# Performance work log

Hardware: AMD Instinct MI355X
Metric: run time of the kernel (lower is better)

Reference implementation:

```python
import jax, jax.numpy as jnp
import numpy as np

LN_EPS = 1e-5


def setup_inputs() -> dict:
    key = jax.random.key(0)
    ks = jax.random.split(key, 8)
    N, E, DIN, DOUT = 50000, 800000, 128, 128
    s = 1.0 / np.sqrt(DIN)
    return {
        "vertex_features": jax.random.normal(ks[0], (N, DIN), jnp.float32),
        "edge_index": jax.random.randint(ks[1], (2, E), 0, N, jnp.int32),
        "W_edge": jax.random.normal(ks[2], (DIN, DOUT), jnp.float32) * s,
        "b_edge": jnp.zeros((DOUT,), jnp.float32),
        "W1": jax.random.normal(ks[3], (DIN + DOUT, DOUT), jnp.float32) * (1.0 / np.sqrt(DIN + DOUT)),
        "b1": jnp.zeros((DOUT,), jnp.float32),
        "ln_gamma": jnp.ones((DOUT,), jnp.float32),
        "ln_beta": jnp.zeros((DOUT,), jnp.float32),
        "W2": jax.random.normal(ks[4], (DOUT, DOUT), jnp.float32) * (1.0 / np.sqrt(DOUT)),
        "b2": jnp.zeros((DOUT,), jnp.float32),
    }


def layer_norm(x, gamma, beta):
    mu = jnp.mean(x, axis=-1, keepdims=True)
    var = jnp.mean(jnp.square(x - mu), axis=-1, keepdims=True)
    return (x - mu) * jax.lax.rsqrt(var + LN_EPS) * gamma + beta


def reference(vertex_features, edge_index, W_edge, b_edge, W1, b1, ln_gamma, ln_beta, W2, b2):
    N = vertex_features.shape[0]
    src, dst = edge_index[0], edge_index[1]
    # gather-subtract: [E, DIN]
    edge_feats = vertex_features[src] - vertex_features[dst]
    # edge linear: [E, DOUT]
    edge_feats = edge_feats @ W_edge + b_edge
    # scatter_max by dst -> [N, DOUT]; empty segments get -inf -> replace with 0
    agg = jax.ops.segment_max(edge_feats, dst, num_segments=N)
    agg = jnp.where(jnp.isfinite(agg), agg, 0.0)
    combined = jnp.concatenate([vertex_features, agg], axis=-1)  # [N, DIN+DOUT]
    h = combined @ W1 + b1
    h = jax.nn.relu(layer_norm(h, ln_gamma, ln_beta))
    return h @ W2 + b2
```

## Files before the change

### kernel.cpp

```cpp
#include <hip/hip_runtime.h>
#include <stdint.h>

#define DIN 128
#define DOUT 128
#define LN_EPS 1e-5f
#define CAP 64

typedef __attribute__((ext_vector_type(8))) short bf16x8;
typedef __attribute__((ext_vector_type(4))) float f32x4;

__device__ __forceinline__ unsigned short f2bf(float f) {
  uint32_t u = __float_as_uint(f);
  uint32_t r = (u + 0x7fffu + ((u >> 16) & 1u)) >> 16;
  return (unsigned short)r;
}
__device__ __forceinline__ float bf2f(uint32_t lo16) {
  return __uint_as_float(lo16 << 16);
}
__device__ __forceinline__ uint32_t pack2(unsigned short a, unsigned short b) {
  return (uint32_t)a | ((uint32_t)b << 16);
}
__device__ __forceinline__ uint32_t cvtpk_bf16(float lo, float hi) {
  uint32_t r;
  asm volatile("v_cvt_pk_bf16_f32 %0, %1, %2" : "=v"(r) : "v"(lo), "v"(hi));
  return r;
}

__global__ __launch_bounds__(256) void k_prep(
    const float* __restrict__ We, const float* __restrict__ W1,
    const float* __restrict__ W2, char* __restrict__ img,
    int4* __restrict__ degv4, int nv4, int wblk) {
  if (blockIdx.x >= wblk) {
    int i = (blockIdx.x - wblk) * 256 + threadIdx.x;
    if (i < nv4) degv4[i] = make_int4(0, 0, 0, 0);
    return;
  }
  int tid = blockIdx.x * 256 + threadIdx.x;
  const int total = 128 * 128 + 256 * 128 + 128 * 128;
  for (int i = tid; i < total; i += wblk * 256) {
    int off;
    float v;
    if (i < 16384) {
      int k = i >> 7, c = i & 127;
      v = We[k * 128 + c];
      off = c * 256 + ((k * 2) ^ ((c & 7) << 4));
    } else if (i < 49152) {
      int j = i - 16384;
      int k = j >> 7, c = j & 127;
      v = W1[k * 128 + c];
      off = 32768 + c * 512 + ((k * 2) ^ ((c & 7) << 4));
    } else {
      int j = i - 49152;
      int k = j >> 7, c = j & 127;
      v = W2[k * 128 + c];
      off = 98304 + c * 256 + ((k * 2) ^ ((c & 7) << 4));
    }
    *(unsigned short*)(img + off) = f2bf(v);
  }
}

__global__ __launch_bounds__(256, 1) void k_gemm_histplace(
    const float* __restrict__ vf, const char* __restrict__ wimg,
    short* __restrict__ P16, short* __restrict__ vf16, int N,
    const int* __restrict__ ei, int* __restrict__ deg,
    unsigned short* __restrict__ ssrc, int E, int nblk) {
  __shared__ char Wet[32768];
  if (blockIdx.x >= nblk) {
    int e = (blockIdx.x - nblk) * 256 + threadIdx.x;
    if (e < E) {
      int s = ei[e];
      int d = ei[E + e];
      int r = atomicAdd(&deg[d], 1);
      if (r < CAP) ssrc[(size_t)d * CAP + r] = (unsigned short)s;
    }
    return;
  }
  {
    const uint4* src = (const uint4*)wimg;
    for (int i = threadIdx.x; i < 2048; i += 256) *(uint4*)(Wet + i * 16) = src[i];
  }
  int wave = threadIdx.x >> 6, lane = threadIdx.x & 63;
  int l15 = lane & 15, lq = lane >> 4;
  int row0 = blockIdx.x * 256 + wave * 64;
  int rs[4];
#pragma unroll
  for (int m = 0; m < 4; ++m) rs[m] = min(row0 + m * 16 + l15, N - 1);

  f32x4 acc[4][8];
#pragma unroll
  for (int m = 0; m < 4; ++m)
#pragma unroll
    for (int n = 0; n < 8; ++n) acc[m][n] = (f32x4)0.f;

  float4 pf0[4], pf1[4];
#pragma unroll
  for (int m = 0; m < 4; ++m) {
    const float* p = vf + (size_t)rs[m] * DIN + lq * 8;
    pf0[m] = *(const float4*)p;
    pf1[m] = *(const float4*)(p + 4);
  }
  __syncthreads();

#pragma unroll
  for (int ks = 0; ks < 4; ++ks) {
    bf16x8 afr[4];
#pragma unroll
    for (int m = 0; m < 4; ++m) {
      uint4 st;
      st.x = cvtpk_bf16(pf0[m].x, pf0[m].y);
      st.y = cvtpk_bf16(pf0[m].z, pf0[m].w);
      st.z = cvtpk_bf16(pf1[m].x, pf1[m].y);
      st.w = cvtpk_bf16(pf1[m].z, pf1[m].w);
      afr[m] = *(bf16x8*)&st;
      int row = row0 + m * 16 + l15;
      if (row < N)
        *(uint4*)(vf16 + (size_t)row * DIN + ks * 32 + lq * 8) = st;
    }
    if (ks < 3) {
#pragma unroll
      for (int m = 0; m < 4; ++m) {
        const float* p = vf + (size_t)rs[m] * DIN + (ks + 1) * 32 + lq * 8;
        pf0[m] = *(const float4*)p;
        pf1[m] = *(const float4*)(p + 4);
      }
    }
    int kb = ks * 64 + lq * 16;
#pragma unroll
    for (int n = 0; n < 8; ++n) {
      int c = n * 16 + l15;
      bf16x8 b = *(const bf16x8*)(Wet + c * 256 + (kb ^ ((c & 7) << 4)));
#pragma unroll
      for (int m = 0; m < 4; ++m)
        acc[m][n] = __builtin_amdgcn_mfma_f32_16x16x32_bf16(afr[m], b, acc[m][n], 0, 0, 0);
    }
  }
#pragma unroll
  for (int m = 0; m < 4; ++m) {
    int rbase = row0 + m * 16 + lq * 4;
#pragma unroll
    for (int n = 0; n < 8; ++n) {
      int col = n * 16 + l15;
#pragma unroll
      for (int reg = 0; reg < 4; ++reg) {
        int row = rbase + reg;
        if (row < N) P16[(size_t)row * DOUT + col] = (short)f2bf(acc[m][n][reg]);
      }
    }
  }
}

__global__ __launch_bounds__(256) void k_segmax(const short* __restrict__ P16,
                                                const int* __restrict__ degA,
                                                const unsigned short* __restrict__ ssrc,
                                                const float* __restrict__ b_edge,
                                                short* __restrict__ A16, int N) {
  int lane = threadIdx.x & 63;
  int l16 = lane & 15;
  int v = blockIdx.x * 16 + (threadIdx.x >> 4);
  if (v >= N) return;
  int deg = min(degA[v], CAP);
  size_t beg = (size_t)v * CAP;
  float m[8];
#pragma unroll
  for (int j = 0; j < 8; ++j) m[j] = -__builtin_inff();
  for (int r = 0; r < deg; r += 16) {
    int cnt = min(16, deg - r);
    int sv = (l16 < cnt) ? (int)ssrc[beg + r + l16] : 0;
#pragma unroll 2
    for (int i = 0; i < cnt; ++i) {
      int s = __shfl(sv, (lane & 48) + i, 64);
      uint4 p = *(const uint4*)(P16 + (size_t)s * DOUT + l16 * 8);
      m[0] = fmaxf(m[0], bf2f(p.x & 0xffffu));
      m[1] = fmaxf(m[1], bf2f(p.x >> 16));
      m[2] = fmaxf(m[2], bf2f(p.y & 0xffffu));
      m[3] = fmaxf(m[3], bf2f(p.y >> 16));
      m[4] = fmaxf(m[4], bf2f(p.z & 0xffffu));
      m[5] = fmaxf(m[5], bf2f(p.z >> 16));
      m[6] = fmaxf(m[6], bf2f(p.w & 0xffffu));
      m[7] = fmaxf(m[7], bf2f(p.w >> 16));
    }
  }
  uint4 pv = *(const uint4*)(P16 + (size_t)v * DOUT + l16 * 8);
  float4 be0 = *(const float4*)(b_edge + l16 * 8);
  float4 be1 = *(const float4*)(b_edge + l16 * 8 + 4);
  float pvf[8] = {bf2f(pv.x & 0xffffu), bf2f(pv.x >> 16), bf2f(pv.y & 0xffffu),
                  bf2f(pv.y >> 16),     bf2f(pv.z & 0xffffu), bf2f(pv.z >> 16),
                  bf2f(pv.w & 0xffffu), bf2f(pv.w >> 16)};
  float bev[8] = {be0.x, be0.y, be0.z, be0.w, be1.x, be1.y, be1.z, be1.w};
  uint32_t o[4];
#pragma unroll
  for (int j = 0; j < 4; ++j) {
    float a0 = (deg > 0) ? (m[2 * j] - pvf[2 * j] + bev[2 * j]) : 0.f;
    float a1 = (deg > 0) ? (m[2 * j + 1] - pvf[2 * j + 1] + bev[2 * j + 1]) : 0.f;
    o[j] = pack2(f2bf(a0), f2bf(a1));
  }
  *(uint4*)(A16 + (size_t)v * DOUT + l16 * 8) = *(uint4*)o;
}

__global__ __launch_bounds__(256, 2) void k_mlp12(
    const short* __restrict__ vf16, const short* __restrict__ A16,
    const char* __restrict__ wimg, const float* __restrict__ b1,
    const float* __restrict__ gamma, const float* __restrict__ beta,
    const float* __restrict__ b2, float* __restrict__ out, int N) {
  __shared__ char lds[65536];
  char* W1h = lds;
  char* W2t = lds + 32768;
  {
    const uint4* wsrc = (const uint4*)wimg;
    for (int i = threadIdx.x; i < 2048; i += 256) {
      int c = i >> 4, x = i & 15;
      ((uint4*)W1h)[i] = wsrc[2048 + c * 32 + x];
      ((uint4*)W2t)[i] = wsrc[6144 + i];
    }
  }
  int wave = threadIdx.x >> 6, lane = threadIdx.x & 63;
  int l15 = lane & 15, lq = lane >> 4;
  int row0 = blockIdx.x * 128 + wave * 32;
  int rs[2];
#pragma unroll
  for (int m = 0; m < 2; ++m) rs[m] = min(row0 + m * 16 + l15, N - 1);
  float b1v[8], gv[8], bev[8], b2v[8];
#pragma unroll
  for (int n = 0; n < 8; ++n) {
    int c = n * 16 + l15;
    b1v[n] = b1[c];
    gv[n] = gamma[c];
    bev[n] = beta[c];
    b2v[n] = b2[c];
  }
  f32x4 acc[2][8];
#pragma unroll
  for (int m = 0; m < 2; ++m)
#pragma unroll
    for (int n = 0; n < 8; ++n) acc[m][n] = (f32x4)0.f;

  uint4 pa[2];
#pragma unroll
  for (int m = 0; m < 2; ++m)
    pa[m] = *(const uint4*)(vf16 + (size_t)rs[m] * DIN + lq * 8);
  __syncthreads();

#pragma unroll
  for (int ks = 0; ks < 8; ++ks) {
    if (ks == 4) {
      __syncthreads();
      const uint4* wsrc = (const uint4*)wimg;
      for (int i = threadIdx.x; i < 2048; i += 256) {
        int c = i >> 4, x = i & 15;
        ((uint4*)W1h)[i] = wsrc[2048 + c * 32 + 16 + x];
      }
      __syncthreads();
    }
    bf16x8 afr[2];
#pragma unroll
    for (int m = 0; m < 2; ++m) afr[m] = *(bf16x8*)&pa[m];
    if (ks < 7) {
      int ks1 = ks + 1;
      const short* srcb = (ks1 < 4) ? vf16 : A16;
      int chunk = (ks1 < 4) ? ks1 : ks1 - 4;
#pragma unroll
      for (int m = 0; m < 2; ++m)
        pa[m] = *(const uint4*)(srcb + (size_t)rs[m] * DIN + chunk * 32 + lq * 8);
    }
    int kb = (ks & 3) * 64 + lq * 16;
#pragma unroll
    for (int n = 0; n < 8; ++n) {
      int c = n * 16 + l15;
      bf16x8 b = *(const bf16x8*)(W1h + c * 256 + (kb ^ ((c & 7) << 4)));
#pragma unroll
      for (int m = 0; m < 2; ++m)
        acc[m][n] = __builtin_amdgcn_mfma_f32_16x16x32_bf16(afr[m], b, acc[m][n], 0, 0, 0);
    }
  }
  __syncthreads();

#pragma unroll
  for (int m = 0; m < 2; ++m) {
#pragma unroll
    for (int n = 0; n < 8; ++n)
#pragma unroll
      for (int reg = 0; reg < 4; ++reg) acc[m][n][reg] += b1v[n];
    float s[4], sq[4];
#pragma unroll
    for (int reg = 0; reg < 4; ++reg) {
      s[reg] = 0.f;
      sq[reg] = 0.f;
#pragma unroll
      for (int n = 0; n < 8; ++n) {
        float h = acc[m][n][reg];
        s[reg] += h;
        sq[reg] += h * h;
      }
    }
#pragma unroll
    for (int mm = 1; mm < 16; mm <<= 1) {
#pragma unroll
      for (int reg = 0; reg < 4; ++reg) {
        s[reg] += __shfl_xor(s[reg], mm, 64);
        sq[reg] += __shfl_xor(sq[reg], mm, 64);
      }
    }
#pragma unroll
    for (int reg = 0; reg < 4; ++reg) {
      float mu = s[reg] * (1.f / 128.f);
      float var = sq[reg] * (1.f / 128.f) - mu * mu;
      float rsn = rsqrtf(var + LN_EPS);
      int rr = wave * 32 + m * 16 + lq * 4 + reg;
#pragma unroll
      for (int n = 0; n < 8; ++n) {
        float o = fmaxf(fmaf((acc[m][n][reg] - mu) * rsn, gv[n], bev[n]), 0.f);
        int c = n * 16 + l15;
        *(unsigned short*)(W1h + rr * 256 + ((c * 2) ^ ((rr & 7) << 4))) = f2bf(o);
      }
    }
  }
  __syncthreads();

  f32x4 acc2[2][8];
#pragma unroll
  for (int m = 0; m < 2; ++m)
#pragma unroll
    for (int n = 0; n < 8; ++n) acc2[m][n] = (f32x4)0.f;
#pragma unroll
  for (int ks = 0; ks < 4; ++ks) {
    int kb = ks * 64 + lq * 16;
    bf16x8 a2[2];
#pragma unroll
    for (int m = 0; m < 2; ++m) {
      int rr = wave * 32 + m * 16 + l15;
      a2[m] = *(const bf16x8*)(W1h + rr * 256 + (kb ^ ((rr & 7) << 4)));
    }
#pragma unroll
    for (int n = 0; n < 8; ++n) {
      int c = n * 16 + l15;
      bf16x8 b = *(const bf16x8*)(W2t + c * 256 + (kb ^ ((c & 7) << 4)));
#pragma unroll
      for (int m = 0; m < 2; ++m)
        acc2[m][n] = __builtin_amdgcn_mfma_f32_16x16x32_bf16(a2[m], b, acc2[m][n], 0, 0, 0);
    }
  }
#pragma unroll
  for (int m = 0; m < 2; ++m) {
    int rbase = row0 + m * 16 + lq * 4;
#pragma unroll
    for (int n = 0; n < 8; ++n) {
      int col = n * 16 + l15;
#pragma unroll
      for (int reg = 0; reg < 4; ++reg) {
        int row = rbase + reg;
        if (row < N) out[(size_t)row * DOUT + col] = acc2[m][n][reg] + b2v[n];
      }
    }
  }
}

extern "C" void kernel_launch(void* const* d_in, const int* in_sizes, int n_in,
                              void* d_out, int out_size, void* d_ws, size_t ws_size,
                              hipStream_t stream) {
  const float* vf     = (const float*)d_in[0];
  const int*   ei     = (const int*)d_in[1];
  const float* W_edge = (const float*)d_in[2];
  const float* b_edge = (const float*)d_in[3];
  const float* W1     = (const float*)d_in[4];
  const float* b1     = (const float*)d_in[5];
  const float* gamma  = (const float*)d_in[6];
  const float* beta   = (const float*)d_in[7];
  const float* W2     = (const float*)d_in[8];
  const float* b2     = (const float*)d_in[9];
  float* out = (float*)d_out;

  int N = in_sizes[0] / DIN;
  int E = in_sizes[1] / 2;
  int nblk = (N + 255) / 256;
  int eblk = (E + 255) / 256;
  int mblk = (N + 127) / 128;

  char* ws = (char*)d_ws;
  size_t seg16 = (size_t)N * DOUT * sizeof(short);
  short* P16  = (short*)ws;
  short* vf16 = (short*)(ws + seg16);
  short* A16  = (short*)(ws + 2 * seg16);
  char*  wimg = ws + 3 * seg16;
  int*   deg  = (int*)(ws + 3 * seg16 + 131072);
  unsigned short* ssrc = (unsigned short*)(deg + ((N + 3) & ~3));

  int nv4 = (N + 3) / 4;
  int zblk = (nv4 + 255) / 256;
  k_prep<<<64 + zblk, 256, 0, stream>>>(W_edge, W1, W2, wimg, (int4*)deg, nv4, 64);
  k_gemm_histplace<<<nblk + eblk, 256, 0, stream>>>(vf, wimg, P16, vf16, N, ei,
                                                    deg, ssrc, E, nblk);
  k_segmax<<<(N + 15) / 16, 256, 0, stream>>>(P16, deg, ssrc, b_edge, A16, N);
  k_mlp12<<<mblk, 256, 0, stream>>>(vf16, A16, wimg, b1, gamma, beta, b2, out, N);
}
```

Measured before the change: 109.3 us.

## Fuse segment-max aggregation into the MLP kernel via shared-memory tile

```diff
diff --git a/kernel.cpp b/kernel.cpp
--- a/kernel.cpp
+++ b/kernel.cpp
@@ -24,6 +24,16 @@
   uint32_t r;
   asm volatile("v_cvt_pk_bf16_f32 %0, %1, %2" : "=v"(r) : "v"(lo), "v"(hi));
   return r;
+}
+__device__ __forceinline__ void max8(float m[8], uint4 p) {
+  m[0] = fmaxf(m[0], bf2f(p.x & 0xffffu));
+  m[1] = fmaxf(m[1], bf2f(p.x >> 16));
+  m[2] = fmaxf(m[2], bf2f(p.y & 0xffffu));
+  m[3] = fmaxf(m[3], bf2f(p.y >> 16));
+  m[4] = fmaxf(m[4], bf2f(p.z & 0xffffu));
+  m[5] = fmaxf(m[5], bf2f(p.z >> 16));
+  m[6] = fmaxf(m[6], bf2f(p.w & 0xffffu));
+  m[7] = fmaxf(m[7], bf2f(p.w >> 16));
 }
 
 __global__ __launch_bounds__(256) void k_prep(
@@ -149,83 +159,86 @@
   }
 }
 
-__global__ __launch_bounds__(256) void k_segmax(const short* __restrict__ P16,
-                                                const int* __restrict__ degA,
-                                                const unsigned short* __restrict__ ssrc,
-                                                const float* __restrict__ b_edge,
-                                                short* __restrict__ A16, int N) {
+__global__ __launch_bounds__(256, 2) void k_segmlp(
+    const short* __restrict__ P16, const short* __restrict__ vf16,
+    const int* __restrict__ degA, const unsigned short* __restrict__ ssrc,
+    const float* __restrict__ b_edge, const char* __restrict__ wimg,
+    const float* __restrict__ b1, const float* __restrict__ gamma,
+    const float* __restrict__ beta, const float* __restrict__ b2,
+    float* __restrict__ out, int N) {
+  __shared__ char lds[65536];
+  char* R0 = lds;
+  char* R1 = lds + 32768;
+  const uint4* wsrc = (const uint4*)wimg;
+
+  int row0 = blockIdx.x * 128;
   int lane = threadIdx.x & 63;
   int l16 = lane & 15;
-  int v = blockIdx.x * 16 + (threadIdx.x >> 4);
-  if (v >= N) return;
-  int deg = min(degA[v], CAP);
-  size_t beg = (size_t)v * CAP;
-  float m[8];
-#pragma unroll
-  for (int j = 0; j < 8; ++j) m[j] = -__builtin_inff();
-  for (int r = 0; r < deg; r += 16) {
-    int cnt = min(16, deg - r);
-    int sv = (l16 < cnt) ? (int)ssrc[beg + r + l16] : 0;
+  int gbase = lane & 48;
+
+  for (int i = threadIdx.x; i < 2048; i += 256) {
+    int c = i >> 4, x = i & 15;
+    ((uint4*)R1)[i] = wsrc[2048 + c * 32 + x];
+  }
+
+  {
+    int grp = threadIdx.x >> 4;
+    float4 be0 = *(const float4*)(b_edge + l16 * 8);
+    float4 be1 = *(const float4*)(b_edge + l16 * 8 + 4);
+    float bev[8] = {be0.x, be0.y, be0.z, be0.w, be1.x, be1.y, be1.z, be1.w};
+#pragma unroll 1
+    for (int k = 0; k < 8; ++k) {
+      int vloc = grp + k * 16;
+      int v = row0 + vloc;
+      uint4 o4 = make_uint4(0, 0, 0, 0);
+      if (v < N) {
+        int deg = min(degA[v], CAP);
+        size_t beg = (size_t)v * CAP;
+        float m[8];
+#pragma unroll
+        for (int j = 0; j < 8; ++j) m[j] = -__builtin_inff();
+        for (int r = 0; r < deg; r += 16) {
+          int cnt = min(16, deg - r);
+          int sv = (l16 < cnt) ? (int)ssrc[beg + r + l16] : 0;
 #pragma unroll 2
-    for (int i = 0; i < cnt; ++i) {
-      int s = __shfl(sv, (lane & 48) + i, 64);
-      uint4 p = *(const uint4*)(P16 + (size_t)s * DOUT + l16 * 8);
-      m[0] = fmaxf(m[0], bf2f(p.x & 0xffffu));
-      m[1] = fmaxf(m[1], bf2f(p.x >> 16));
-      m[2] = fmaxf(m[2], bf2f(p.y & 0xffffu));
-      m[3] = fmaxf(m[3], bf2f(p.y >> 16));
-      m[4] = fmaxf(m[4], bf2f(p.z & 0xffffu));
-      m[5] = fmaxf(m[5], bf2f(p.z >> 16));
-      m[6] = fmaxf(m[6], bf2f(p.w & 0xffffu));
-      m[7] = fmaxf(m[7], bf2f(p.w >> 16));
-    }
-  }
-  uint4 pv = *(const uint4*)(P16 + (size_t)v * DOUT + l16 * 8);
-  float4 be0 = *(const float4*)(b_edge + l16 * 8);
-  float4 be1 = *(const float4*)(b_edge + l16 * 8 + 4);
-  float pvf[8] = {bf2f(pv.x & 0xffffu), bf2f(pv.x >> 16), bf2f(pv.y & 0xffffu),
-                  bf2f(pv.y >> 16),     bf2f(pv.z & 0xffffu), bf2f(pv.z >> 16),
-                  bf2f(pv.w & 0xffffu), bf2f(pv.w >> 16)};
-  float bev[8] = {be0.x, be0.y, be0.z, be0.w, be1.x, be1.y, be1.z, be1.w};
-  uint32_t o[4];
-#pragma unroll
-  for (int j = 0; j < 4; ++j) {
-    float a0 = (deg > 0) ? (m[2 * j] - pvf[2 * j] + bev[2 * j]) : 0.f;
-    float a1 = (deg > 0) ? (m[2 * j + 1] - pvf[2 * j + 1] + bev[2 * j + 1]) : 0.f;
-    o[j] = pack2(f2bf(a0), f2bf(a1));
-  }
-  *(uint4*)(A16 + (size_t)v * DOUT + l16 * 8) = *(uint4*)o;
-}
-
-__global__ __launch_bounds__(256, 2) void k_mlp12(
-    const short* __restrict__ vf16, const short* __restrict__ A16,
-    const char* __restrict__ wimg, const float* __restrict__ b1,
-    const float* __restrict__ gamma, const float* __restrict__ beta,
-    const float* __restrict__ b2, float* __restrict__ out, int N) {
-  __shared__ char lds[65536];
-  char* W1h = lds;
-  char* W2t = lds + 32768;
-  {
-    const uint4* wsrc = (const uint4*)wimg;
-    for (int i = threadIdx.x; i < 2048; i += 256) {
-      int c = i >> 4, x = i & 15;
-      ((uint4*)W1h)[i] = wsrc[2048 + c * 32 + x];
-      ((uint4*)W2t)[i] = wsrc[6144 + i];
-    }
-  }
-  int wave = threadIdx.x >> 6, lane = threadIdx.x & 63;
+          for (int i = 0; i < cnt; ++i) {
+            int s = __shfl(sv, gbase + i, 64);
+            uint4 p = *(const uint4*)(P16 + (size_t)s * DOUT + l16 * 8);
+            max8(m, p);
+          }
+        }
+        if (deg > 0) {
+          uint4 pv = *(const uint4*)(P16 + (size_t)v * DOUT + l16 * 8);
+          float pvf[8] = {bf2f(pv.x & 0xffffu), bf2f(pv.x >> 16),
+                          bf2f(pv.y & 0xffffu), bf2f(pv.y >> 16),
+                          bf2f(pv.z & 0xffffu), bf2f(pv.z >> 16),
+                          bf2f(pv.w & 0xffffu), bf2f(pv.w >> 16)};
+          uint32_t o[4];
+#pragma unroll
+          for (int j = 0; j < 4; ++j)
+            o[j] = pack2(f2bf(m[2 * j] - pvf[2 * j] + bev[2 * j]),
+                         f2bf(m[2 * j + 1] - pvf[2 * j + 1] + bev[2 * j + 1]));
+          o4 = *(uint4*)o;
+        }
+      }
+      if (vloc < 128)
+        *(uint4*)(R0 + vloc * 256 + ((l16 * 16) ^ ((vloc & 7) << 4))) = o4;
+    }
+  }
+  __syncthreads();
+
+  int wave = threadIdx.x >> 6;
   int l15 = lane & 15, lq = lane >> 4;
-  int row0 = blockIdx.x * 128 + wave * 32;
   int rs[2];
 #pragma unroll
-  for (int m = 0; m < 2; ++m) rs[m] = min(row0 + m * 16 + l15, N - 1);
-  float b1v[8], gv[8], bev[8], b2v[8];
+  for (int m = 0; m < 2; ++m) rs[m] = min(row0 + wave * 32 + m * 16 + l15, N - 1);
+  float b1v[8], gv[8], bevn[8], b2v[8];
 #pragma unroll
   for (int n = 0; n < 8; ++n) {
     int c = n * 16 + l15;
     b1v[n] = b1[c];
     gv[n] = gamma[c];
-    bev[n] = beta[c];
+    bevn[n] = beta[c];
     b2v[n] = b2[c];
   }
   f32x4 acc[2][8];
@@ -238,41 +251,56 @@
 #pragma unroll
   for (int m = 0; m < 2; ++m)
     pa[m] = *(const uint4*)(vf16 + (size_t)rs[m] * DIN + lq * 8);
-  __syncthreads();
-
-#pragma unroll
-  for (int ks = 0; ks < 8; ++ks) {
-    if (ks == 4) {
-      __syncthreads();
-      const uint4* wsrc = (const uint4*)wimg;
-      for (int i = threadIdx.x; i < 2048; i += 256) {
-        int c = i >> 4, x = i & 15;
-        ((uint4*)W1h)[i] = wsrc[2048 + c * 32 + 16 + x];
-      }
-      __syncthreads();
-    }
+
+#pragma unroll
+  for (int ks = 0; ks < 4; ++ks) {
     bf16x8 afr[2];
 #pragma unroll
     for (int m = 0; m < 2; ++m) afr[m] = *(bf16x8*)&pa[m];
-    if (ks < 7) {
-      int ks1 = ks + 1;
-      const short* srcb = (ks1 < 4) ? vf16 : A16;
-      int chunk = (ks1 < 4) ? ks1 : ks1 - 4;
+    if (ks < 3) {
 #pragma unroll
       for (int m = 0; m < 2; ++m)
-        pa[m] = *(const uint4*)(srcb + (size_t)rs[m] * DIN + chunk * 32 + lq * 8);
-    }
-    int kb = (ks & 3) * 64 + lq * 16;
+        pa[m] = *(const uint4*)(vf16 + (size_t)rs[m] * DIN + (ks + 1) * 32 + lq * 8);
+    }
+    int kb = ks * 64 + lq * 16;
 #pragma unroll
     for (int n = 0; n < 8; ++n) {
       int c = n * 16 + l15;
-      bf16x8 b = *(const bf16x8*)(W1h + c * 256 + (kb ^ ((c & 7) << 4)));
+      bf16x8 b = *(const bf16x8*)(R1 + c * 256 + (kb ^ ((c & 7) << 4)));
 #pragma unroll
       for (int m = 0; m < 2; ++m)
         acc[m][n] = __builtin_amdgcn_mfma_f32_16x16x32_bf16(afr[m], b, acc[m][n], 0, 0, 0);
     }
   }
   __syncthreads();
+  for (int i = threadIdx.x; i < 2048; i += 256) {
+    int c = i >> 4, x = i & 15;
+    ((uint4*)R1)[i] = wsrc[2048 + c * 32 + 16 + x];
+  }
+  __syncthreads();
+
+#pragma unroll
+  for (int ks = 0; ks < 4; ++ks) {
+    int kb = ks * 64 + lq * 16;
+    bf16x8 afr[2];
+#pragma unroll
+    for (int m = 0; m < 2; ++m) {
+      int rr = wave * 32 + m * 16 + l15;
+      afr[m] = *(const bf16x8*)(R0 + rr * 256 + (kb ^ ((rr & 7) << 4)));
+    }
+#pragma unroll
+    for (int n = 0; n < 8; ++n) {
+      int c = n * 16 + l15;
+      bf16x8 b = *(const bf16x8*)(R1 + c * 256 + (kb ^ ((c & 7) << 4)));
+#pragma unroll
+      for (int m = 0; m < 2; ++m)
+        acc[m][n] = __builtin_amdgcn_mfma_f32_16x16x32_bf16(afr[m], b, acc[m][n], 0, 0, 0);
+    }
+  }
+  __syncthreads();
+
+  for (int i = threadIdx.x; i < 2048; i += 256)
+    ((uint4*)R0)[i] = wsrc[6144 + i];
 
 #pragma unroll
   for (int m = 0; m < 2; ++m) {
@@ -308,9 +336,9 @@
       int rr = wave * 32 + m * 16 + lq * 4 + reg;
 #pragma unroll
       for (int n = 0; n < 8; ++n) {
-        float o = fmaxf(fmaf((acc[m][n][reg] - mu) * rsn, gv[n], bev[n]), 0.f);
+        float o = fmaxf(fmaf((acc[m][n][reg] - mu) * rsn, gv[n], bevn[n]), 0.f);
         int c = n * 16 + l15;
-        *(unsigned short*)(W1h + rr * 256 + ((c * 2) ^ ((rr & 7) << 4))) = f2bf(o);
+        *(unsigned short*)(R1 + rr * 256 + ((c * 2) ^ ((rr & 7) << 4))) = f2bf(o);
       }
     }
   }
@@ -328,12 +356,12 @@
 #pragma unroll
     for (int m = 0; m < 2; ++m) {
       int rr = wave * 32 + m * 16 + l15;
-      a2[m] = *(const bf16x8*)(W1h + rr * 256 + (kb ^ ((rr & 7) << 4)));
+      a2[m] = *(const bf16x8*)(R1 + rr * 256 + (kb ^ ((rr & 7) << 4)));
     }
 #pragma unroll
     for (int n = 0; n < 8; ++n) {
       int c = n * 16 + l15;
-      bf16x8 b = *(const bf16x8*)(W2t + c * 256 + (kb ^ ((c & 7) << 4)));
+      bf16x8 b = *(const bf16x8*)(R0 + c * 256 + (kb ^ ((c & 7) << 4)));
 #pragma unroll
       for (int m = 0; m < 2; ++m)
         acc2[m][n] = __builtin_amdgcn_mfma_f32_16x16x32_bf16(a2[m], b, acc2[m][n], 0, 0, 0);
@@ -341,7 +369,7 @@
   }
 #pragma unroll
   for (int m = 0; m < 2; ++m) {
-    int rbase = row0 + m * 16 + lq * 4;
+    int rbase = row0 + wave * 32 + m * 16 + lq * 4;
 #pragma unroll
     for (int n = 0; n < 8; ++n) {
       int col = n * 16 + l15;
@@ -379,9 +407,8 @@
   size_t seg16 = (size_t)N * DOUT * sizeof(short);
   short* P16  = (short*)ws;
   short* vf16 = (short*)(ws + seg16);
-  short* A16  = (short*)(ws + 2 * seg16);
-  char*  wimg = ws + 3 * seg16;
-  int*   deg  = (int*)(ws + 3 * seg16 + 131072);
+  char*  wimg = ws + 2 * seg16;
+  int*   deg  = (int*)(ws + 2 * seg16 + 131072);
   unsigned short* ssrc = (unsigned short*)(deg + ((N + 3) & ~3));
 
   int nv4 = (N + 3) / 4;
@@ -389,6 +416,6 @@
   k_prep<<<64 + zblk, 256, 0, stream>>>(W_edge, W1, W2, wimg, (int4*)deg, nv4, 64);
   k_gemm_histplace<<<nblk + eblk, 256, 0, stream>>>(vf, wimg, P16, vf16, N, ei,
                                                     deg, ssrc, E, nblk);
-  k_segmax<<<(N + 15) / 16, 256, 0, stream>>>(P16, deg, ssrc, b_edge, A16, N);
-  k_mlp12<<<mblk, 256, 0, stream>>>(vf16, A16, wimg, b1, gamma, beta, b2, out, N);
-}
+  k_segmlp<<<mblk, 256, 0, stream>>>(P16, vf16, deg, ssrc, b_edge, wimg, b1,
+                                     gamma, beta, b2, out, N);
+}
```

New measurement: 157.5 us. 1.44x slower.
